# Performance work log

Measured on AMD Instinct MI355X. Metric: run time of the kernel, lower is better.

## Reference

```python
import jax, jax.numpy as jnp
import numpy as np

B, R, K, C, H, E = 256, 6, 49, 512, 1024, 300
NV, NR, NL = 504, 190, 2001


def setup_inputs() -> dict:
    key = jax.random.key(0)
    ks = list(jax.random.split(key, 40))
    it = iter(ks)

    def nrm(shape, s=0.02):
        return jax.random.normal(next(it), shape, jnp.float32) * s

    return dict(
        v_org=jax.random.normal(next(it), (B, C, 7, 7), jnp.float32),
        img_feat=jax.random.normal(next(it), (B, K, C), jnp.float32),
        gt_verb=jax.random.randint(next(it), (B,), 0, NV),
        role_idx=jax.random.randint(next(it), (B, R), 0, NR),
        mask=jnp.ones((B, R, R), jnp.int32),
        verb_table=nrm((NV, E)),
        role_table=nrm((NR, E)),
        qc_W=nrm((2 * E, H)), qc_b=jnp.zeros((H,), jnp.float32),
        av_W=nrm((C, H)), av_b=jnp.zeros((H,), jnp.float32),
        aq_W=nrm((H, H)), aq_b=jnp.zeros((H,), jnp.float32),
        ao_W=nrm((H, 1)), ao_b=jnp.zeros((1,), jnp.float32),
        vn_W=nrm((C, H)), vn_b=jnp.zeros((H,), jnp.float32),
        qn_W=nrm((H, H)), qn_b=jnp.zeros((H,), jnp.float32),
        Wq=nrm((H, H)), Wk=nrm((H, H)), Wv=nrm((H, H)), Wo=nrm((H, H)),
        uqc_W=nrm((H + 2 * E, H)), uqc_b=jnp.zeros((H,), jnp.float32),
        cls_W=nrm((H, NL)), cls_b=jnp.zeros((NL,), jnp.float32),
    )


def _mfb(q_repr, v_repr):
    # elementwise MFB pool (n_heads=1 -> sumpool is identity), sign-sqrt, L2 norm
    z = q_repr * v_repr
    s = jnp.sqrt(jax.nn.relu(z)) - jnp.sqrt(jax.nn.relu(-z))
    n = jnp.sqrt(jnp.sum(s * s, axis=1, keepdims=True))
    return s / jnp.maximum(n, 1e-12)


def _v_att(img, q_emb, av_W, av_b, aq_W, aq_b, ao_W, ao_b):
    v = jax.nn.relu(img @ av_W + av_b)            # [N,K,H]
    q = jax.nn.relu(q_emb @ aq_W + aq_b)          # [N,H]
    logits = (v * q[:, None, :]) @ ao_W + ao_b    # [N,K,1]
    return jax.nn.softmax(logits, axis=1)


def reference(v_org, img_feat, gt_verb, role_idx, mask, verb_table, role_table,
              qc_W, qc_b, av_W, av_b, aq_W, aq_b, ao_W, ao_b,
              vn_W, vn_b, qn_W, qn_b, Wq, Wk, Wv, Wo,
              uqc_W, uqc_b, cls_W, cls_b):
    Bn, Cn, h, w = v_org.shape
    Rn = role_idx.shape[1]
    img0 = v_org.reshape(Bn, Cn, h * w).transpose(0, 2, 1)          # [B,K,C]
    img = jnp.broadcast_to(img0[:, None], (Bn, Rn, h * w, Cn)).reshape(Bn * Rn, h * w, Cn)
    Kv, Cv = img_feat.shape[1], img_feat.shape[2]
    img_v = jnp.broadcast_to(img_feat[:, None], (Bn, Rn, Kv, Cv)).reshape(Bn * Rn, Kv, Cv)

    verb_e = verb_table[gt_verb]                                     # [B,E]
    role_e = role_table[role_idx]                                    # [B,R,E]
    rv = jnp.concatenate([jnp.broadcast_to(verb_e[:, None], (Bn, Rn, verb_e.shape[-1])), role_e], -1)
    rv = rv.reshape(Bn * Rn, -1)                                     # [BR,2E]

    q_emb = jax.nn.relu(rv @ qc_W + qc_b)

    att = _v_att(img, q_emb, av_W, av_b, aq_W, aq_b, ao_W, ao_b)
    v_emb = (att * img).sum(1)
    v_repr = jax.nn.relu(v_emb @ vn_W + vn_b)
    q_repr = jax.nn.relu(q_emb @ qn_W + qn_b)
    out = _mfb(q_repr, v_repr)
    ans0 = out

    att_v = _v_att(img_v, q_emb, av_W, av_b, aq_W, aq_b, ao_W, ao_b)
    v_repr_verb = jax.nn.relu((att_v * img_v).sum(1) @ vn_W + vn_b)
    out_verb = _mfb(q_repr, v_repr_verb)

    # masked neighbour attention over role nodes (single head)
    Hd = out.shape[-1]
    cur = out.reshape(Bn, Rn, Hd)
    qh, kh, vh = cur @ Wq, cur @ Wk, cur @ Wv
    scores = jnp.einsum('bid,bjd->bij', qh, kh) / jnp.sqrt(jnp.float32(Hd))
    m = mask.astype(jnp.float32) * (1.0 - jnp.eye(Rn, dtype=jnp.float32))  # no self edges
    scores = jnp.where(m > 0, scores, jnp.float32(-1e9))
    attn = jax.nn.softmax(scores, axis=-1)
    neigh = (jnp.einsum('bij,bjd->bid', attn, vh) @ Wo).reshape(Bn * Rn, Hd)

    uq = jax.nn.relu(jnp.concatenate([neigh, rv], -1) @ uqc_W + uqc_b)
    att2 = _v_att(img, uq, av_W, av_b, aq_W, aq_b, ao_W, ao_b)
    v_repr2 = jax.nn.relu((att2 * img).sum(1) @ vn_W + vn_b)
    q_repr2 = jax.nn.relu(uq @ qn_W + qn_b)
    out2 = _mfb(q_repr2, v_repr2)

    gate = jax.nn.sigmoid(out2 + out_verb)
    out_f = (1.0 - gate) * out_verb + gate * jnp.tanh(out2 + ans0)

    logits = out_f @ cls_W + cls_b
    return logits.reshape(Bn, Rn, -1)
```

## Files before the change

kernel.cpp:

```cpp
#include <hip/hip_runtime.h>
#include <math.h>

typedef unsigned short u16;
typedef __attribute__((ext_vector_type(8))) short short8;
typedef __attribute__((ext_vector_type(4))) float f32x4;

#define Bb 256
#define Rr 6
#define Ksp 49
#define Cc 512
#define Hh 1024
#define Ee 300
#define NN (Bb*Rr)
#define NLl 2001

__device__ __forceinline__ u16 f2b(float x) {
    union { float f; unsigned u; } c; c.f = x;
    unsigned r = c.u + 0x7fffu + ((c.u >> 16) & 1u);
    return (u16)(r >> 16);
}
__device__ __forceinline__ float b2f(u16 b) {
    union { unsigned u; float f; } c; c.u = ((unsigned)b) << 16; return c.f;
}

#define ASYNC16(gp, lp) __builtin_amdgcn_global_load_lds( \
    (const __attribute__((address_space(1))) unsigned int*)(gp), \
    (__attribute__((address_space(3))) unsigned int*)(lp), 16, 0, 0)

constexpr size_t O_QC   = 0;
constexpr size_t O_AV   = O_QC   + (size_t)1024*608;
constexpr size_t O_AQQN = O_AV   + (size_t)1024*512;
constexpr size_t O_VN   = O_AQQN + (size_t)2048*1024;
constexpr size_t O_QKV  = O_VN   + (size_t)1024*512;
constexpr size_t O_WO   = O_QKV  + (size_t)3072*1024;
constexpr size_t O_UQC  = O_WO   + (size_t)1024*1024;
constexpr size_t O_CLS  = O_UQC  + (size_t)1024*1632;
constexpr size_t WT_ELEMS = O_CLS + (size_t)2048*1024;

template<int WM, int WN>
__global__ void __launch_bounds__(256) gemm_bf16(
    const u16* __restrict__ A, int lda, const u16* __restrict__ Bt,
    const float* __restrict__ bias,
    u16* __restrict__ Cb, int ldcb, float* __restrict__ Cf, int ldcf,
    int N, int K, int split, int Nreal, int act)
{
    constexpr int SM = 2 * WM, SN = 2 * WN;
    constexpr int BM = 16 * SM, BN = 16 * SN;
    constexpr int APW = SM / 4 > 0 ? SM / 4 : 1;
    constexpr int BPW = SN / 4 > 0 ? SN / 4 : 1;
    __shared__ u16 lds[(SM + SN) * 64 * 8];
    const int tid  = threadIdx.x;
    const int wave = tid >> 6, lane = tid & 63;
    const int m0 = lane & 15, q0 = lane >> 4;
    const int bm = blockIdx.y * BM, bn = blockIdx.x * BN;
    const int wr = wave >> 1, wc = wave & 1;

    f32x4 acc[WM][WN];
    #pragma unroll
    for (int i = 0; i < WM; i++)
        #pragma unroll
        for (int j = 0; j < WN; j++)
            acc[i][j] = (f32x4){0.f, 0.f, 0.f, 0.f};

    for (int kt = 0; kt < K; kt += 32) {
        #pragma unroll
        for (int i = 0; i < APW; i++) {
            const int s = wave * APW + i;
            const u16* g = A + (size_t)(bm + s * 16 + m0) * lda + kt + q0 * 8;
            ASYNC16(g, &lds[(s * 64) * 8]);
        }
        #pragma unroll
        for (int i = 0; i < BPW; i++) {
            const int s = wave * BPW + i;
            const u16* g = Bt + (size_t)(bn + s * 16 + m0) * K + kt + q0 * 8;
            ASYNC16(g, &lds[((SM + s) * 64) * 8]);
        }
        __syncthreads();
        short8 af[WM], bfr[WN];
        #pragma unroll
        for (int i = 0; i < WM; i++)
            af[i] = *(const short8*)&lds[((wr * WM + i) * 64 + lane) * 8];
        #pragma unroll
        for (int j = 0; j < WN; j++)
            bfr[j] = *(const short8*)&lds[((SM + wc * WN + j) * 64 + lane) * 8];
        #pragma unroll
        for (int i = 0; i < WM; i++)
            #pragma unroll
            for (int j = 0; j < WN; j++)
                acc[i][j] = __builtin_amdgcn_mfma_f32_16x16x32_bf16(
                    af[i], bfr[j], acc[i][j], 0, 0, 0);
        __syncthreads();
    }

    #pragma unroll
    for (int i = 0; i < WM; i++) {
        #pragma unroll
        for (int j = 0; j < WN; j++) {
            const int col = bn + (wc * WN + j) * 16 + m0;
            if (col >= Nreal) continue;
            const float bv = bias ? bias[col] : 0.f;
            #pragma unroll
            for (int r = 0; r < 4; r++) {
                const int row = bm + (wr * WM + i) * 16 + q0 * 4 + r;
                float v = acc[i][j][r] + bv;
                if (act) v = fmaxf(v, 0.f);
                if (col < split) Cb[(size_t)row * ldcb + col] = f2b(v);
                else             Cf[(size_t)row * ldcf + col - split] = v;
            }
        }
    }
}

struct PrepSrc { const float* s[11]; };

__global__ void __launch_bounds__(256) prep_kernel(
    PrepSrc ps, u16* __restrict__ wt,
    const float* __restrict__ verb_table, const float* __restrict__ role_table,
    const int* __restrict__ gt_verb, const int* __restrict__ role_idx,
    u16* __restrict__ cat,
    const float* __restrict__ v_org, u16* __restrict__ A1,
    const float* __restrict__ img_feat, u16* __restrict__ A2,
    const float* __restrict__ aq_b, const float* __restrict__ qn_b,
    float* __restrict__ aqqn_b)
{
    __shared__ float sm[64 * 50];
    const int bid = blockIdx.x, tid = threadIdx.x;

    if (bid < 11456) {
        const int tStart[12] = {0,608,1120,2144,3168,3680,4704,5728,6752,7776,9408,11456};
        const int tK[11]  = {600,512,1024,1024,512,1024,1024,1024,1024,1624,1024};
        const int tN[11]  = {1024,1024,1024,1024,1024,1024,1024,1024,1024,1024,2001};
        const int tKp[11] = {608,512,1024,1024,512,1024,1024,1024,1024,1632,1024};
        const int tNp[11] = {1024,1024,1024,1024,1024,1024,1024,1024,1024,1024,2048};
        const long tDst[11] = {(long)O_QC,(long)O_AV,(long)O_AQQN,(long)(O_AQQN+1048576),
                               (long)O_VN,(long)O_QKV,(long)(O_QKV+1048576),
                               (long)(O_QKV+2097152),(long)O_WO,(long)O_UQC,(long)O_CLS};
        int e = 0;
        while (bid >= tStart[e + 1]) e++;
        const int local = bid - tStart[e];
        const int ktiles = tKp[e] >> 5;
        const int bx = local % ktiles, by = local / ktiles;
        const float* W = ps.s[e];
        u16* Wt = wt + tDst[e];
        const int K = tK[e], Nn = tN[e], Kp = tKp[e], Np = tNp[e];
        const int kt = bx * 32, nt = by * 32;
        const int tx = tid & 31, ty = tid >> 5;
        for (int i = ty; i < 32; i += 8) {
            const int k = kt + i, n = nt + tx;
            sm[i * 33 + tx] = (k < K && n < Nn) ? W[(size_t)k * Nn + n] : 0.f;
        }
        __syncthreads();
        for (int i = ty; i < 32; i += 8) {
            const int n = nt + i, k = kt + tx;
            if (n < Np && k < Kp) Wt[(size_t)n * Kp + k] = f2b(sm[tx * 33 + i]);
        }
    } else if (bid < 15104) {
        const int idx = (bid - 11456) * 256 + tid;
        const int n = idx / 608;
        const int col = idx - n * 608;
        const int b = n / Rr, r = n - b * Rr;
        float v = 0.f;
        if (col < Ee)          v = verb_table[(size_t)gt_verb[b] * Ee + col];
        else if (col < 2 * Ee) v = role_table[(size_t)role_idx[b * Rr + r] * Ee + (col - Ee)];
        cat[(size_t)n * 1632 + 1024 + col] = f2b(v);
    } else if (bid < 17152) {
        const int local = bid - 15104;
        const int b = local >> 3, c0 = (local & 7) << 6;
        {
            const int ci = tid >> 2, k0 = tid & 3;
            const float* p = v_org + ((size_t)b * Cc + c0 + ci) * Ksp;
            for (int k = k0; k < Ksp; k += 4) sm[ci * 50 + k] = p[k];
        }
        __syncthreads();
        {
            const int cc = tid & 63, kb = tid >> 6;
            for (int k = kb; k < Ksp; k += 4)
                A1[((size_t)b * Ksp + k) * Cc + c0 + cc] = f2b(sm[cc * 50 + k]);
        }
    } else if (bid < 23424) {
        const int i = (bid - 17152) * 256 + tid;
        const float4 v = ((const float4*)img_feat)[i];
        ushort4 o;
        o.x = f2b(v.x); o.y = f2b(v.y); o.z = f2b(v.z); o.w = f2b(v.w);
        ((ushort4*)A2)[i] = o;
    } else {
        const int i = (bid - 23424) * 256 + tid;
        if (i < 2048) aqqn_b[i] = (i < 1024) ? aq_b[i] : qn_b[i - 1024];
    }
}

__global__ void __launch_bounds__(256) att_kernel(
    const u16* __restrict__ Vh,
    const u16* __restrict__ Q,
    const float* __restrict__ aoW, const float* __restrict__ aoB,
    const u16* __restrict__ IMGb,
    u16* __restrict__ Vemb)
{
    const int b = blockIdx.x;
    const int tid = threadIdx.x, wave = tid >> 6, lane = tid & 63;
    __shared__ u16 s_qs[16][1032];
    __shared__ float s_log[64][6];
    __shared__ float s_att[49][6];

    for (int n = 0; n < 16; n++) {
        const u16* qp = Q + ((size_t)b * Rr + n) * Hh;
        for (int h = tid; h < 1032; h += 256) {
            u16 v = 0;
            if (n < Rr && h < Hh) v = f2b(b2f(qp[h]) * aoW[h]);
            s_qs[n][h] = v;
        }
    }
    __syncthreads();

    const int m = lane & 15, q = lane >> 4;
    {
        f32x4 acc = (f32x4){0.f, 0.f, 0.f, 0.f};
        const u16* arow = Vh + ((size_t)b * Ksp + wave * 16 + m) * Hh + q * 8;
        const u16* brow = &s_qs[m][q * 8];
        for (int kt = 0; kt < Hh; kt += 32) {
            const short8 af = *(const short8*)(arow + kt);
            const short8 bf = *(const short8*)(brow + kt);
            acc = __builtin_amdgcn_mfma_f32_16x16x32_bf16(af, bf, acc, 0, 0, 0);
        }
        const float aob = aoB[0];
        #pragma unroll
        for (int r = 0; r < 4; r++) {
            const int k = wave * 16 + q * 4 + r;
            if (k < Ksp && m < Rr) s_log[k][m] = acc[r] + aob;
        }
    }
    __syncthreads();

    if (wave == 0) {
        for (int r = 0; r < Rr; r++) {
            const float v = (lane < Ksp) ? s_log[lane][r] : -INFINITY;
            float mx = v;
            #pragma unroll
            for (int off = 32; off; off >>= 1) mx = fmaxf(mx, __shfl_down(mx, off));
            mx = __shfl(mx, 0);
            const float e = (lane < Ksp) ? expf(v - mx) : 0.f;
            float s = e;
            #pragma unroll
            for (int off = 32; off; off >>= 1) s += __shfl_down(s, off);
            s = __shfl(s, 0);
            if (lane < Ksp) s_att[lane][r] = e / s;
        }
    }
    __syncthreads();

    float acc2[Rr][2];
    #pragma unroll
    for (int r = 0; r < Rr; r++) { acc2[r][0] = 0.f; acc2[r][1] = 0.f; }
    const u16* ib = IMGb + (size_t)b * Ksp * Cc + tid * 2;
    #pragma unroll 7
    for (int k = 0; k < Ksp; k++) {
        const ushort2 v = *(const ushort2*)(ib + (size_t)k * Cc);
        const float v0 = b2f(v.x), v1 = b2f(v.y);
        #pragma unroll
        for (int r = 0; r < Rr; r++) {
            const float w = s_att[k][r];
            acc2[r][0] += w * v0; acc2[r][1] += w * v1;
        }
    }
    #pragma unroll
    for (int r = 0; r < Rr; r++) {
        ushort2 o; o.x = f2b(acc2[r][0]); o.y = f2b(acc2[r][1]);
        *(ushort2*)(Vemb + ((size_t)b * Rr + r) * Cc + tid * 2) = o;
    }
}

__global__ void __launch_bounds__(256) mfb_kernel(
    const float* __restrict__ q, const float* __restrict__ v,
    float* __restrict__ outf, u16* __restrict__ outb)
{
    const int n = blockIdx.x;
    const int tid = threadIdx.x;
    __shared__ float red[4];
    float sv[4];
    float local = 0.f;
    #pragma unroll
    for (int i = 0; i < 4; i++) {
        const int h = tid + i * 256;
        const float z = q[(size_t)n * Hh + h] * v[(size_t)n * Hh + h];
        const float s = (z > 0.f) ? sqrtf(z) : -sqrtf(-z);
        sv[i] = s;
        local += s * s;
    }
    #pragma unroll
    for (int off = 32; off; off >>= 1) local += __shfl_down(local, off);
    if ((tid & 63) == 0) red[tid >> 6] = local;
    __syncthreads();
    const float tot = red[0] + red[1] + red[2] + red[3];
    const float inv = 1.f / fmaxf(sqrtf(tot), 1e-12f);
    #pragma unroll
    for (int i = 0; i < 4; i++) {
        const float o = sv[i] * inv;
        const size_t off2 = (size_t)n * Hh + tid + i * 256;
        outf[off2] = o;
        if (outb) outb[off2] = f2b(o);
    }
}

__global__ void __launch_bounds__(256) mfb_gate_kernel(
    const float* __restrict__ q, const float* __restrict__ v,
    const float* __restrict__ ovb, const float* __restrict__ oa0,
    u16* __restrict__ outb)
{
    const int n = blockIdx.x;
    const int tid = threadIdx.x;
    __shared__ float red[4];
    float sv[4];
    float local = 0.f;
    #pragma unroll
    for (int i = 0; i < 4; i++) {
        const int h = tid + i * 256;
        const float z = q[(size_t)n * Hh + h] * v[(size_t)n * Hh + h];
        const float s = (z > 0.f) ? sqrtf(z) : -sqrtf(-z);
        sv[i] = s;
        local += s * s;
    }
    #pragma unroll
    for (int off = 32; off; off >>= 1) local += __shfl_down(local, off);
    if ((tid & 63) == 0) red[tid >> 6] = local;
    __syncthreads();
    const float tot = red[0] + red[1] + red[2] + red[3];
    const float inv = 1.f / fmaxf(sqrtf(tot), 1e-12f);
    #pragma unroll
    for (int i = 0; i < 4; i++) {
        const size_t off2 = (size_t)n * Hh + tid + i * 256;
        const float o2 = sv[i] * inv;
        const float ov = ovb[off2], a0 = oa0[off2];
        const float g = 1.f / (1.f + expf(-(o2 + ov)));
        outb[off2] = f2b((1.f - g) * ov + g * tanhf(o2 + a0));
    }
}

__global__ void __launch_bounds__(256) nattn_kernel(
    const float* __restrict__ qkv, const int* __restrict__ mask,
    u16* __restrict__ nv)
{
    const int b = blockIdx.x;
    const int tid = threadIdx.x;
    __shared__ float s_sc[Rr][Rr];
    __shared__ float s_at[Rr][Rr];
    const int wave = tid >> 6, lane = tid & 63;
    for (int p = wave; p < Rr * Rr; p += 4) {
        const int i = p / Rr, j = p - (p / Rr) * Rr;
        const float* qp = qkv + ((size_t)(b * Rr + i)) * 3072;
        const float* kp = qkv + ((size_t)(b * Rr + j)) * 3072 + 1024;
        float s = 0.f;
        for (int h = lane; h < Hh; h += 64) s += qp[h] * kp[h];
        #pragma unroll
        for (int off = 32; off; off >>= 1) s += __shfl_down(s, off);
        if (lane == 0) s_sc[i][j] = s * 0.03125f;
    }
    __syncthreads();
    if (tid < Rr) {
        const int i = tid;
        float vals[Rr];
        float m = -INFINITY;
        #pragma unroll
        for (int j = 0; j < Rr; j++) {
            const float mij = (i == j) ? 0.f : (float)mask[b * Rr * Rr + i * Rr + j];
            const float v = (mij > 0.f) ? s_sc[i][j] : -1e9f;
            vals[j] = v;
            m = fmaxf(m, v);
        }
        float ssum = 0.f;
        #pragma unroll
        for (int j = 0; j < Rr; j++) { const float e = expf(vals[j] - m); s_at[i][j] = e; ssum += e; }
        const float invs = 1.f / ssum;
        #pragma unroll
        for (int j = 0; j < Rr; j++) s_at[i][j] *= invs;
    }
    __syncthreads();
    for (int h = tid; h < Hh; h += 256) {
        #pragma unroll
        for (int i = 0; i < Rr; i++) {
            float acc = 0.f;
            #pragma unroll
            for (int j = 0; j < Rr; j++)
                acc += s_at[i][j] * qkv[((size_t)(b * Rr + j)) * 3072 + 2048 + h];
            nv[((size_t)(b * Rr + i)) * Hh + h] = f2b(acc);
        }
    }
}

extern "C" void kernel_launch(void* const* d_in, const int* in_sizes, int n_in,
                              void* d_out, int out_size, void* d_ws, size_t ws_size,
                              hipStream_t stream)
{
    const float* v_org      = (const float*)d_in[0];
    const float* img_feat   = (const float*)d_in[1];
    const int*   gt_verb    = (const int*)d_in[2];
    const int*   role_idx   = (const int*)d_in[3];
    const int*   mask       = (const int*)d_in[4];
    const float* verb_table = (const float*)d_in[5];
    const float* role_table = (const float*)d_in[6];
    const float* qc_W  = (const float*)d_in[7];
    const float* qc_b  = (const float*)d_in[8];
    const float* av_W  = (const float*)d_in[9];
    const float* av_b  = (const float*)d_in[10];
    const float* aq_W  = (const float*)d_in[11];
    const float* aq_b  = (const float*)d_in[12];
    const float* ao_W  = (const float*)d_in[13];
    const float* ao_b  = (const float*)d_in[14];
    const float* vn_W  = (const float*)d_in[15];
    const float* vn_b  = (const float*)d_in[16];
    const float* qn_W  = (const float*)d_in[17];
    const float* qn_b  = (const float*)d_in[18];
    const float* Wq    = (const float*)d_in[19];
    const float* Wk    = (const float*)d_in[20];
    const float* Wv    = (const float*)d_in[21];
    const float* Wo    = (const float*)d_in[22];
    const float* uqc_W = (const float*)d_in[23];
    const float* uqc_b = (const float*)d_in[24];
    const float* cls_W = (const float*)d_in[25];
    const float* cls_b = (const float*)d_in[26];
    float* out = (float*)d_out;

    char* base = (char*)d_ws;
    size_t off = 0;
    auto alloc = [&](size_t bytes) -> char* {
        char* p = base + off;
        off += (bytes + 255) & ~(size_t)255;
        return p;
    };
    u16* wt = (u16*)alloc(WT_ELEMS * 2);
    u16* A1 = (u16*)alloc((size_t)12544 * 512 * 2 * 2);
    u16* A2 = A1 + (size_t)12544 * 512;
    u16* v_img  = (u16*)alloc((size_t)12544 * 1024 * 2);
    char* P2    = alloc((size_t)12544 * 1024 * 2);
    u16* v_imgv = (u16*)P2;
    u16* nv     = (u16*)P2;
    float* qkv  = (float*)(P2 + 3145728);
    u16* uq     = (u16*)(P2 + 3145728);
    u16* out_f  = (u16*)(P2 + 6291456);
    u16* cat    = (u16*)alloc((size_t)NN * 1632 * 2);
    u16* q_emb  = (u16*)alloc((size_t)NN * 1024 * 2);
    u16* q_att  = (u16*)alloc((size_t)NN * 1024 * 2);
    u16* v_emb  = (u16*)alloc((size_t)NN * 512 * 2);
    float* q_rep = (float*)alloc((size_t)NN * 1024 * 4);
    float* v_rep = (float*)alloc((size_t)NN * 1024 * 4);
    float* a0f   = (float*)alloc((size_t)NN * 1024 * 4);
    u16*   a0b   = (u16*)alloc((size_t)NN * 1024 * 2);
    float* vbf   = (float*)alloc((size_t)NN * 1024 * 4);
    float* aqqn_b = (float*)alloc(2048 * 4);

    const dim3 blk(256);

    PrepSrc ps;
    ps.s[0] = qc_W;  ps.s[1] = av_W; ps.s[2] = aq_W; ps.s[3] = qn_W;
    ps.s[4] = vn_W;  ps.s[5] = Wq;   ps.s[6] = Wk;   ps.s[7] = Wv;
    ps.s[8] = Wo;    ps.s[9] = uqc_W; ps.s[10] = cls_W;
    prep_kernel<<<dim3(23432), blk, 0, stream>>>(
        ps, wt, verb_table, role_table, gt_verb, role_idx, cat,
        v_org, A1, img_feat, A2, aq_b, qn_b, aqqn_b);

    gemm_bf16<2,2><<<dim3(16, 24), blk, 0, stream>>>(
        cat + 1024, 1632, wt + O_QC, qc_b, q_emb, 1024, nullptr, 0,
        1024, 608, 1024, 1024, 1);
    gemm_bf16<4,4><<<dim3(8, 196), blk, 0, stream>>>(
        A1, 512, wt + O_AV, av_b, v_img, 1024, nullptr, 0,
        1024, 512, 1024, 1024, 1);
    gemm_bf16<2,2><<<dim3(32, 24), blk, 0, stream>>>(
        q_emb, 1024, wt + O_AQQN, aqqn_b, q_att, 1024, q_rep, 1024,
        2048, 1024, 1024, 2048, 1);
    att_kernel<<<dim3(Bb), blk, 0, stream>>>(v_img, q_att, ao_W, ao_b, A1, v_emb);
    gemm_bf16<2,2><<<dim3(16, 24), blk, 0, stream>>>(
        v_emb, 512, wt + O_VN, vn_b, nullptr, 0, v_rep, 1024,
        1024, 512, 0, 1024, 1);
    mfb_kernel<<<dim3(NN), blk, 0, stream>>>(q_rep, v_rep, a0f, a0b);
    att_kernel<<<dim3(Bb), blk, 0, stream>>>(v_imgv, q_att, ao_W, ao_b, A2, v_emb);
    gemm_bf16<2,2><<<dim3(16, 24), blk, 0, stream>>>(
        v_emb, 512, wt + O_VN, vn_b, nullptr, 0, v_rep, 1024,
        1024, 512, 0, 1024, 1);
    mfb_kernel<<<dim3(NN), blk, 0, stream>>>(q_rep, v_rep, vbf, nullptr);
    gemm_bf16<2,2><<<dim3(48, 24), blk, 0, stream>>>(
        a0b, 1024, wt + O_QKV, nullptr, nullptr, 0, qkv, 3072,
        3072, 1024, 0, 3072, 0);
    nattn_kernel<<<dim3(Bb), blk, 0, stream>>>(qkv, mask, nv);
    gemm_bf16<2,2><<<dim3(16, 24), blk, 0, stream>>>(
        nv, 1024, wt + O_WO, nullptr, cat, 1632, nullptr, 0,
        1024, 1024, 1024, 1024, 0);
    gemm_bf16<2,2><<<dim3(16, 24), blk, 0, stream>>>(
        cat, 1632, wt + O_UQC, uqc_b, uq, 1024, nullptr, 0,
        1024, 1632, 1024, 1024, 1);
    gemm_bf16<2,2><<<dim3(32, 24), blk, 0, stream>>>(
        uq, 1024, wt + O_AQQN, aqqn_b, q_att, 1024, q_rep, 1024,
        2048, 1024, 1024, 2048, 1);
    att_kernel<<<dim3(Bb), blk, 0, stream>>>(v_img, q_att, ao_W, ao_b, A1, v_emb);
    gemm_bf16<2,2><<<dim3(16, 24), blk, 0, stream>>>(
        v_emb, 512, wt + O_VN, vn_b, nullptr, 0, v_rep, 1024,
        1024, 512, 0, 1024, 1);
    mfb_gate_kernel<<<dim3(NN), blk, 0, stream>>>(q_rep, v_rep, vbf, a0f, out_f);
    gemm_bf16<2,2><<<dim3(32, 24), blk, 0, stream>>>(
        out_f, 1024, wt + O_CLS, cls_b, nullptr, 0, out, 2001,
        2048, 1024, 0, 2001, 0);
}
```

Baseline: 619.3 us.

## Batch verb and role attention branches and retile GEMMs with BK=64

The GEMM template now takes block M, N and K sizes, so each 32-step K loop can load two sub-tiles per barrier. K dimensions are padded to 640 and 1664 to fit the deeper tile. The 1536-row GEMMs switch to 32x64 tiles, giving twice as many blocks, which should fill the GPU better. The two independent attention passes (image and img_feat) now run as one 512-block att_kernel, one VN GEMM over 3072 rows and one merged mfb2 kernel. This removes launches and serialization, at the cost of more scratch memory and a larger LDS footprint per block.

```diff
diff --git a/kernel.cpp b/kernel.cpp
--- a/kernel.cpp
+++ b/kernel.cpp
@@ -28,27 +28,26 @@
     (__attribute__((address_space(3))) unsigned int*)(lp), 16, 0, 0)
 
 constexpr size_t O_QC   = 0;
-constexpr size_t O_AV   = O_QC   + (size_t)1024*608;
+constexpr size_t O_AV   = O_QC   + (size_t)1024*640;
 constexpr size_t O_AQQN = O_AV   + (size_t)1024*512;
 constexpr size_t O_VN   = O_AQQN + (size_t)2048*1024;
 constexpr size_t O_QKV  = O_VN   + (size_t)1024*512;
 constexpr size_t O_WO   = O_QKV  + (size_t)3072*1024;
 constexpr size_t O_UQC  = O_WO   + (size_t)1024*1024;
-constexpr size_t O_CLS  = O_UQC  + (size_t)1024*1632;
+constexpr size_t O_CLS  = O_UQC  + (size_t)1024*1664;
 constexpr size_t WT_ELEMS = O_CLS + (size_t)2048*1024;
 
-template<int WM, int WN>
+template<int BM, int BN, int BK>
 __global__ void __launch_bounds__(256) gemm_bf16(
     const u16* __restrict__ A, int lda, const u16* __restrict__ Bt,
     const float* __restrict__ bias,
     u16* __restrict__ Cb, int ldcb, float* __restrict__ Cf, int ldcf,
-    int N, int K, int split, int Nreal, int act)
-{
-    constexpr int SM = 2 * WM, SN = 2 * WN;
-    constexpr int BM = 16 * SM, BN = 16 * SN;
-    constexpr int APW = SM / 4 > 0 ? SM / 4 : 1;
-    constexpr int BPW = SN / 4 > 0 ? SN / 4 : 1;
-    __shared__ u16 lds[(SM + SN) * 64 * 8];
+    int K, int split, int Nreal, int act)
+{
+    constexpr int SM = BM / 16, SN = BN / 16;
+    constexpr int KG = BK / 32;
+    constexpr int WM = BM / 32, WN = BN / 32;
+    __shared__ u16 lds[(SM + SN) * KG * 512];
     const int tid  = threadIdx.x;
     const int wave = tid >> 6, lane = tid & 63;
     const int m0 = lane & 15, q0 = lane >> 4;
@@ -62,33 +61,41 @@
         for (int j = 0; j < WN; j++)
             acc[i][j] = (f32x4){0.f, 0.f, 0.f, 0.f};
 
-    for (int kt = 0; kt < K; kt += 32) {
-        #pragma unroll
-        for (int i = 0; i < APW; i++) {
-            const int s = wave * APW + i;
-            const u16* g = A + (size_t)(bm + s * 16 + m0) * lda + kt + q0 * 8;
-            ASYNC16(g, &lds[(s * 64) * 8]);
-        }
-        #pragma unroll
-        for (int i = 0; i < BPW; i++) {
-            const int s = wave * BPW + i;
-            const u16* g = Bt + (size_t)(bn + s * 16 + m0) * K + kt + q0 * 8;
-            ASYNC16(g, &lds[((SM + s) * 64) * 8]);
-        }
+    for (int kt = 0; kt < K; kt += BK) {
+        #pragma unroll
+        for (int s = wave; s < SM; s += 4)
+            #pragma unroll
+            for (int g = 0; g < KG; g++) {
+                const u16* gp = A + (size_t)(bm + s * 16 + m0) * lda + kt + g * 32 + q0 * 8;
+                ASYNC16(gp, &lds[(s * KG + g) * 512]);
+            }
+        #pragma unroll
+        for (int s = wave; s < SN; s += 4)
+            #pragma unroll
+            for (int g = 0; g < KG; g++) {
+                const u16* gp = Bt + (size_t)(bn + s * 16 + m0) * K + kt + g * 32 + q0 * 8;
+                ASYNC16(gp, &lds[(SM * KG + s * KG + g) * 512]);
+            }
         __syncthreads();
-        short8 af[WM], bfr[WN];
+        short8 af[WM][KG], bf[WN][KG];
         #pragma unroll
         for (int i = 0; i < WM; i++)
-            af[i] = *(const short8*)&lds[((wr * WM + i) * 64 + lane) * 8];
+            #pragma unroll
+            for (int g = 0; g < KG; g++)
+                af[i][g] = *(const short8*)&lds[(((wr * WM + i) * KG + g) * 64 + lane) * 8];
         #pragma unroll
         for (int j = 0; j < WN; j++)
-            bfr[j] = *(const short8*)&lds[((SM + wc * WN + j) * 64 + lane) * 8];
-        #pragma unroll
-        for (int i = 0; i < WM; i++)
-            #pragma unroll
-            for (int j = 0; j < WN; j++)
-                acc[i][j] = __builtin_amdgcn_mfma_f32_16x16x32_bf16(
-                    af[i], bfr[j], acc[i][j], 0, 0, 0);
+            #pragma unroll
+            for (int g = 0; g < KG; g++)
+                bf[j][g] = *(const short8*)&lds[((SM * KG + (wc * WN + j) * KG + g) * 64 + lane) * 8];
+        #pragma unroll
+        for (int g = 0; g < KG; g++)
+            #pragma unroll
+            for (int i = 0; i < WM; i++)
+                #pragma unroll
+                for (int j = 0; j < WN; j++)
+                    acc[i][j] = __builtin_amdgcn_mfma_f32_16x16x32_bf16(
+                        af[i][g], bf[j][g], acc[i][j], 0, 0, 0);
         __syncthreads();
     }
 
@@ -126,11 +133,11 @@
     __shared__ float sm[64 * 50];
     const int bid = blockIdx.x, tid = threadIdx.x;
 
-    if (bid < 11456) {
-        const int tStart[12] = {0,608,1120,2144,3168,3680,4704,5728,6752,7776,9408,11456};
+    if (bid < 11520) {
+        const int tStart[12] = {0,640,1152,2176,3200,3712,4736,5760,6784,7808,9472,11520};
         const int tK[11]  = {600,512,1024,1024,512,1024,1024,1024,1024,1624,1024};
         const int tN[11]  = {1024,1024,1024,1024,1024,1024,1024,1024,1024,1024,2001};
-        const int tKp[11] = {608,512,1024,1024,512,1024,1024,1024,1024,1632,1024};
+        const int tKp[11] = {640,512,1024,1024,512,1024,1024,1024,1024,1664,1024};
         const int tNp[11] = {1024,1024,1024,1024,1024,1024,1024,1024,1024,1024,2048};
         const long tDst[11] = {(long)O_QC,(long)O_AV,(long)O_AQQN,(long)(O_AQQN+1048576),
                                (long)O_VN,(long)O_QKV,(long)(O_QKV+1048576),
@@ -154,17 +161,17 @@
             const int n = nt + i, k = kt + tx;
             if (n < Np && k < Kp) Wt[(size_t)n * Kp + k] = f2b(sm[tx * 33 + i]);
         }
-    } else if (bid < 15104) {
-        const int idx = (bid - 11456) * 256 + tid;
-        const int n = idx / 608;
-        const int col = idx - n * 608;
+    } else if (bid < 15360) {
+        const int idx = (bid - 11520) * 256 + tid;
+        const int n = idx / 640;
+        const int col = idx - n * 640;
         const int b = n / Rr, r = n - b * Rr;
         float v = 0.f;
         if (col < Ee)          v = verb_table[(size_t)gt_verb[b] * Ee + col];
         else if (col < 2 * Ee) v = role_table[(size_t)role_idx[b * Rr + r] * Ee + (col - Ee)];
-        cat[(size_t)n * 1632 + 1024 + col] = f2b(v);
-    } else if (bid < 17152) {
-        const int local = bid - 15104;
+        cat[(size_t)n * 1664 + 1024 + col] = f2b(v);
+    } else if (bid < 17408) {
+        const int local = bid - 15360;
         const int b = local >> 3, c0 = (local & 7) << 6;
         {
             const int ci = tid >> 2, k0 = tid & 3;
@@ -177,26 +184,30 @@
             for (int k = kb; k < Ksp; k += 4)
                 A1[((size_t)b * Ksp + k) * Cc + c0 + cc] = f2b(sm[cc * 50 + k]);
         }
-    } else if (bid < 23424) {
-        const int i = (bid - 17152) * 256 + tid;
+    } else if (bid < 23680) {
+        const int i = (bid - 17408) * 256 + tid;
         const float4 v = ((const float4*)img_feat)[i];
         ushort4 o;
         o.x = f2b(v.x); o.y = f2b(v.y); o.z = f2b(v.z); o.w = f2b(v.w);
         ((ushort4*)A2)[i] = o;
     } else {
-        const int i = (bid - 23424) * 256 + tid;
+        const int i = (bid - 23680) * 256 + tid;
         if (i < 2048) aqqn_b[i] = (i < 1024) ? aq_b[i] : qn_b[i - 1024];
     }
 }
 
 __global__ void __launch_bounds__(256) att_kernel(
-    const u16* __restrict__ Vh,
+    const u16* __restrict__ Vh0,
     const u16* __restrict__ Q,
     const float* __restrict__ aoW, const float* __restrict__ aoB,
-    const u16* __restrict__ IMGb,
-    u16* __restrict__ Vemb)
-{
-    const int b = blockIdx.x;
+    const u16* __restrict__ IMG0,
+    u16* __restrict__ Vemb0)
+{
+    const int task = blockIdx.x >> 8;
+    const int b = blockIdx.x & 255;
+    const u16* Vh   = Vh0   + (size_t)task * 12544 * 1024;
+    const u16* IMGb = IMG0  + (size_t)task * 12544 * 512;
+    u16* Vemb       = Vemb0 + (size_t)task * NN * 512;
     const int tid = threadIdx.x, wave = tid >> 6, lane = tid & 63;
     __shared__ u16 s_qs[16][1032];
     __shared__ float s_log[64][6];
@@ -269,11 +280,12 @@
     }
 }
 
-__global__ void __launch_bounds__(256) mfb_kernel(
+__global__ void __launch_bounds__(256) mfb2_kernel(
     const float* __restrict__ q, const float* __restrict__ v,
-    float* __restrict__ outf, u16* __restrict__ outb)
+    float* __restrict__ a0f, u16* __restrict__ a0b, float* __restrict__ vbf)
 {
     const int n = blockIdx.x;
+    const int qrow = (n < NN) ? n : n - NN;
     const int tid = threadIdx.x;
     __shared__ float red[4];
     float sv[4];
@@ -281,7 +293,7 @@
     #pragma unroll
     for (int i = 0; i < 4; i++) {
         const int h = tid + i * 256;
-        const float z = q[(size_t)n * Hh + h] * v[(size_t)n * Hh + h];
+        const float z = q[(size_t)qrow * Hh + h] * v[(size_t)n * Hh + h];
         const float s = (z > 0.f) ? sqrtf(z) : -sqrtf(-z);
         sv[i] = s;
         local += s * s;
@@ -295,9 +307,12 @@
     #pragma unroll
     for (int i = 0; i < 4; i++) {
         const float o = sv[i] * inv;
-        const size_t off2 = (size_t)n * Hh + tid + i * 256;
-        outf[off2] = o;
-        if (outb) outb[off2] = f2b(o);
+        if (n < NN) {
+            const size_t off2 = (size_t)n * Hh + tid + i * 256;
+            a0f[off2] = o; a0b[off2] = f2b(o);
+        } else {
+            vbf[(size_t)(n - NN) * Hh + tid + i * 256] = o;
+        }
     }
 }
 
@@ -429,19 +444,18 @@
     u16* wt = (u16*)alloc(WT_ELEMS * 2);
     u16* A1 = (u16*)alloc((size_t)12544 * 512 * 2 * 2);
     u16* A2 = A1 + (size_t)12544 * 512;
-    u16* v_img  = (u16*)alloc((size_t)12544 * 1024 * 2);
-    char* P2    = alloc((size_t)12544 * 1024 * 2);
-    u16* v_imgv = (u16*)P2;
-    u16* nv     = (u16*)P2;
-    float* qkv  = (float*)(P2 + 3145728);
-    u16* uq     = (u16*)(P2 + 3145728);
-    u16* out_f  = (u16*)(P2 + 6291456);
-    u16* cat    = (u16*)alloc((size_t)NN * 1632 * 2);
+    u16* v_img = (u16*)alloc((size_t)12544 * 1024 * 2 * 2);
+    u16* v_imgv = v_img + (size_t)12544 * 1024;
+    float* qkv = (float*)v_imgv;
+    u16* nv    = (u16*)((char*)v_imgv + (size_t)NN * 3072 * 4);
+    u16* cat    = (u16*)alloc((size_t)NN * 1664 * 2);
     u16* q_emb  = (u16*)alloc((size_t)NN * 1024 * 2);
     u16* q_att  = (u16*)alloc((size_t)NN * 1024 * 2);
-    u16* v_emb  = (u16*)alloc((size_t)NN * 512 * 2);
+    u16* uq     = (u16*)alloc((size_t)NN * 1024 * 2);
+    u16* out_f  = (u16*)alloc((size_t)NN * 1024 * 2);
+    u16* v_emb2 = (u16*)alloc((size_t)2 * NN * 512 * 2);
+    float* v_rep2 = (float*)alloc((size_t)2 * NN * 1024 * 4);
     float* q_rep = (float*)alloc((size_t)NN * 1024 * 4);
-    float* v_rep = (float*)alloc((size_t)NN * 1024 * 4);
     float* a0f   = (float*)alloc((size_t)NN * 1024 * 4);
     u16*   a0b   = (u16*)alloc((size_t)NN * 1024 * 2);
     float* vbf   = (float*)alloc((size_t)NN * 1024 * 4);
@@ -453,48 +467,43 @@
     ps.s[0] = qc_W;  ps.s[1] = av_W; ps.s[2] = aq_W; ps.s[3] = qn_W;
     ps.s[4] = vn_W;  ps.s[5] = Wq;   ps.s[6] = Wk;   ps.s[7] = Wv;
     ps.s[8] = Wo;    ps.s[9] = uqc_W; ps.s[10] = cls_W;
-    prep_kernel<<<dim3(23432), blk, 0, stream>>>(
+    prep_kernel<<<dim3(23688), blk, 0, stream>>>(
         ps, wt, verb_table, role_table, gt_verb, role_idx, cat,
         v_org, A1, img_feat, A2, aq_b, qn_b, aqqn_b);
 
-    gemm_bf16<2,2><<<dim3(16, 24), blk, 0, stream>>>(
-        cat + 1024, 1632, wt + O_QC, qc_b, q_emb, 1024, nullptr, 0,
-        1024, 608, 1024, 1024, 1);
-    gemm_bf16<4,4><<<dim3(8, 196), blk, 0, stream>>>(
+    gemm_bf16<32,64,64><<<dim3(16, 48), blk, 0, stream>>>(
+        cat + 1024, 1664, wt + O_QC, qc_b, q_emb, 1024, nullptr, 0,
+        640, 1024, 1024, 1);
+    gemm_bf16<128,128,64><<<dim3(8, 196), blk, 0, stream>>>(
         A1, 512, wt + O_AV, av_b, v_img, 1024, nullptr, 0,
-        1024, 512, 1024, 1024, 1);
-    gemm_bf16<2,2><<<dim3(32, 24), blk, 0, stream>>>(
+        512, 1024, 1024, 1);
+    gemm_bf16<32,64,64><<<dim3(32, 48), blk, 0, stream>>>(
         q_emb, 1024, wt + O_AQQN, aqqn_b, q_att, 1024, q_rep, 1024,
-        2048, 1024, 1024, 2048, 1);
-    att_kernel<<<dim3(Bb), blk, 0, stream>>>(v_img, q_att, ao_W, ao_b, A1, v_emb);
-    gemm_bf16<2,2><<<dim3(16, 24), blk, 0, stream>>>(
-        v_emb, 512, wt + O_VN, vn_b, nullptr, 0, v_rep, 1024,
-        1024, 512, 0, 1024, 1);
-    mfb_kernel<<<dim3(NN), blk, 0, stream>>>(q_rep, v_rep, a0f, a0b);
-    att_kernel<<<dim3(Bb), blk, 0, stream>>>(v_imgv, q_att, ao_W, ao_b, A2, v_emb);
-    gemm_bf16<2,2><<<dim3(16, 24), blk, 0, stream>>>(
-        v_emb, 512, wt + O_VN, vn_b, nullptr, 0, v_rep, 1024,
-        1024, 512, 0, 1024, 1);
-    mfb_kernel<<<dim3(NN), blk, 0, stream>>>(q_rep, v_rep, vbf, nullptr);
-    gemm_bf16<2,2><<<dim3(48, 24), blk, 0, stream>>>(
+        1024, 1024, 2048, 1);
+    att_kernel<<<dim3(512), blk, 0, stream>>>(v_img, q_att, ao_W, ao_b, A1, v_emb2);
+    gemm_bf16<32,64,64><<<dim3(16, 96), blk, 0, stream>>>(
+        v_emb2, 512, wt + O_VN, vn_b, nullptr, 0, v_rep2, 1024,
+        512, 0, 1024, 1);
+    mfb2_kernel<<<dim3(2 * NN), blk, 0, stream>>>(q_rep, v_rep2, a0f, a0b, vbf);
+    gemm_bf16<32,64,64><<<dim3(48, 48), blk, 0, stream>>>(
         a0b, 1024, wt + O_QKV, nullptr, nullptr, 0, qkv, 3072,
-        3072, 1024, 0, 3072, 0);
+        1024, 0, 3072, 0);
     nattn_kernel<<<dim3(Bb), blk, 0, stream>>>(qkv, mask, nv);
-    gemm_bf16<2,2><<<dim3(16, 24), blk, 0, stream>>>(
-        nv, 1024, wt + O_WO, nullptr, cat, 1632, nullptr, 0,
-        1024, 1024, 1024, 1024, 0);
-    gemm_bf16<2,2><<<dim3(16, 24), blk, 0, stream>>>(
-        cat, 1632, wt + O_UQC, uqc_b, uq, 1024, nullptr, 0,
-        1024, 1632, 1024, 1024, 1);
-    gemm_bf16<2,2><<<dim3(32, 24), blk, 0, stream>>>(
+    gemm_bf16<32,64,64><<<dim3(16, 48), blk, 0, stream>>>(
+        nv, 1024, wt + O_WO, nullptr, cat, 1664, nullptr, 0,
+        1024, 1024, 1024, 0);
+    gemm_bf16<32,64,64><<<dim3(16, 48), blk, 0, stream>>>(
+        cat, 1664, wt + O_UQC, uqc_b, uq, 1024, nullptr, 0,
+        1664, 1024, 1024, 1);
+    gemm_bf16<32,64,64><<<dim3(32, 48), blk, 0, stream>>>(
         uq, 1024, wt + O_AQQN, aqqn_b, q_att, 1024, q_rep, 1024,
-        2048, 1024, 1024, 2048, 1);
-    att_kernel<<<dim3(Bb), blk, 0, stream>>>(v_img, q_att, ao_W, ao_b, A1, v_emb);
-    gemm_bf16<2,2><<<dim3(16, 24), blk, 0, stream>>>(
-        v_emb, 512, wt + O_VN, vn_b, nullptr, 0, v_rep, 1024,
-        1024, 512, 0, 1024, 1);
-    mfb_gate_kernel<<<dim3(NN), blk, 0, stream>>>(q_rep, v_rep, vbf, a0f, out_f);
-    gemm_bf16<2,2><<<dim3(32, 24), blk, 0, stream>>>(
+        1024, 1024, 2048, 1);
+    att_kernel<<<dim3(Bb), blk, 0, stream>>>(v_img, q_att, ao_W, ao_b, A1, v_emb2);
+    gemm_bf16<32,64,64><<<dim3(16, 48), blk, 0, stream>>>(
+        v_emb2, 512, wt + O_VN, vn_b, nullptr, 0, v_rep2, 1024,
+        512, 0, 1024, 1);
+    mfb_gate_kernel<<<dim3(NN), blk, 0, stream>>>(q_rep, v_rep2, vbf, a0f, out_f);
+    gemm_bf16<32,64,64><<<dim3(32, 48), blk, 0, stream>>>(
         out_f, 1024, wt + O_CLS, cls_b, nullptr, 0, out, 2001,
-        2048, 1024, 0, 2001, 0);
-}
+        1024, 0, 2001, 0);
+}
```

After: 629.9 us. Within noise of the previous version (+1.7%).
